# Performance work log

Measured on AMD Instinct MI355X. Metric: run time of the kernel, lower is better.

Reference implementation:

```python
import jax, jax.numpy as jnp
import numpy as np

N_NODES = 100000
N_EDGES = 600000
DIM_IN = 128
DIM_H = 128
DIM_OUT = 64
N_LAYERS = 3
BN_EPS = 1e-5


def setup_inputs() -> dict:
    key = jax.random.key(0)
    ks = jax.random.split(key, 10)
    x = jax.random.normal(ks[0], (N_NODES, DIM_IN), dtype=jnp.float32)
    edge_index = jax.random.randint(ks[1], (2, N_EDGES), 0, N_NODES, dtype=jnp.int64)
    s = 0.05
    conv_w1 = jax.random.normal(ks[2], (N_LAYERS, DIM_H, DIM_H), dtype=jnp.float32) * s
    conv_b1 = jnp.zeros((N_LAYERS, DIM_H), jnp.float32)
    conv_w2 = jax.random.normal(ks[3], (N_LAYERS, DIM_H, DIM_H), dtype=jnp.float32) * s
    conv_b2 = jnp.zeros((N_LAYERS, DIM_H), jnp.float32)
    bn_gamma = jnp.ones((N_LAYERS, DIM_H), jnp.float32)
    bn_beta = jnp.zeros((N_LAYERS, DIM_H), jnp.float32)
    fc1_w = jax.random.normal(ks[4], (DIM_H, DIM_H), dtype=jnp.float32) * s
    fc1_b = jnp.zeros((DIM_H,), jnp.float32)
    fc2_w = jax.random.normal(ks[5], (DIM_H, DIM_OUT), dtype=jnp.float32) * s
    fc2_b = jnp.zeros((DIM_OUT,), jnp.float32)
    # deterministic dropout mask, p=0.5, inverted-dropout scaling baked in (0 or 2)
    dropout_mask = (jax.random.uniform(ks[6], (N_NODES, DIM_H)) < 0.5).astype(jnp.float32) * 2.0
    return {"x": x, "edge_index": edge_index,
            "conv_w1": conv_w1, "conv_b1": conv_b1, "conv_w2": conv_w2, "conv_b2": conv_b2,
            "bn_gamma": bn_gamma, "bn_beta": bn_beta,
            "fc1_w": fc1_w, "fc1_b": fc1_b, "fc2_w": fc2_w, "fc2_b": fc2_b,
            "dropout_mask": dropout_mask}


def reference(x, edge_index, conv_w1, conv_b1, conv_w2, conv_b2,
              bn_gamma, bn_beta, fc1_w, fc1_b, fc2_w, fc2_b, dropout_mask):
    src, dst = edge_index[0], edge_index[1]
    n = x.shape[0]
    h = x
    for l in range(N_LAYERS):
        # GINConv (eps=0): (1+eps)*h + sum_{j->i} h_j, then 2-layer MLP
        agg = h + jax.ops.segment_sum(h[src], dst, num_segments=n)
        z = jnp.maximum(agg @ conv_w1[l] + conv_b1[l], 0.0) @ conv_w2[l] + conv_b2[l]
        z = jnp.maximum(z, 0.0)  # outer ReLU
        # BatchNorm1d (training mode: batch stats, biased variance)
        mean = z.mean(axis=0)
        var = z.var(axis=0)
        h = (z - mean) * jax.lax.rsqrt(var + BN_EPS) * bn_gamma[l] + bn_beta[l]
    h = jnp.maximum(h @ fc1_w + fc1_b, 0.0)
    h = h * dropout_mask  # dropout p=0.5 with precomputed inverted mask
    logits = h @ fc2_w + fc2_b
    return jax.nn.log_softmax(logits, axis=-1)
```

## Files before the change

kernel.cpp:

```cpp
#include <hip/hip_runtime.h>
#include <stdint.h>

#define N_NODES 100000
#define N_EDGES 600000
#define DIM_H   128
#define DIM_OUT 64
#define WPAD    136
#define BN_EPS  1e-5f
#define NBLK    391
#define GRID64_HEAD 1563
#define MLP_GRID 782

typedef __attribute__((ext_vector_type(8))) __bf16        bh8;
typedef __attribute__((ext_vector_type(4))) float         fl4;
typedef __attribute__((ext_vector_type(8))) unsigned short us8;
typedef __attribute__((ext_vector_type(4))) unsigned short us4;

__device__ __forceinline__ unsigned short f2bfbits(float f) {
  unsigned int u = __builtin_bit_cast(unsigned int, f);
  u += 0x7fffu + ((u >> 16) & 1u);
  return (unsigned short)(u >> 16);
}
__device__ __forceinline__ float bf2f(unsigned short b) {
  unsigned int u = ((unsigned int)b) << 16;
  return __builtin_bit_cast(float, u);
}
__device__ __forceinline__ void wave_lds_fence() {
  asm volatile("s_waitcnt lgkmcnt(0)" ::: "memory");
  __builtin_amdgcn_sched_barrier(0);
}

__global__ void prep_kernel(const float* __restrict__ cw1, const float* __restrict__ cw2,
                            const float* __restrict__ fc1w, const float* __restrict__ fc2w,
                            unsigned short* __restrict__ W1F, unsigned short* __restrict__ W2F,
                            unsigned short* __restrict__ F1F, unsigned short* __restrict__ F2F,
                            float* __restrict__ stats, int* __restrict__ deg,
                            unsigned short* __restrict__ zrow) {
  int t = blockIdx.x * 256 + threadIdx.x;
  if (t < 3 * 16384) {
    int l = t >> 14, o = t & 16383;
    int j = o & 7, lane = (o >> 3) & 63, kk = (o >> 9) & 3, n0 = o >> 11;
    int k = kk * 32 + ((lane >> 4) << 3) + j;
    int n = (n0 << 4) + (lane & 15);
    W1F[t] = f2bfbits(cw1[l * 16384 + k * 128 + n]);
    W2F[t] = f2bfbits(cw2[l * 16384 + k * 128 + n]);
  }
  if (t < 16384) {
    int o = t;
    int j = o & 7, lane = (o >> 3) & 63, kk = (o >> 9) & 3, n0 = o >> 11;
    int k = kk * 32 + ((lane >> 4) << 3) + j;
    int n = (n0 << 4) + (lane & 15);
    F1F[t] = f2bfbits(fc1w[k * 128 + n]);
  }
  if (t < 8192) {
    int o = t;
    int j = o & 7, lane = (o >> 3) & 63, kk = (o >> 9) & 3, n0 = o >> 11;
    int k = kk * 32 + ((lane >> 4) << 3) + j;
    int n = (n0 << 4) + (lane & 15);
    F2F[t] = f2bfbits(fc2w[k * 64 + n]);
  }
  if (t < 6144)  stats[t] = 0.f;
  if (t < 128)   zrow[t] = 0;
  if (t < N_NODES) deg[t] = 0;
}

__global__ void deg_xcast(const float* __restrict__ x, unsigned short* __restrict__ xB,
                          const int* __restrict__ ei, int* __restrict__ deg,
                          const float* __restrict__ mask, unsigned int* __restrict__ bmask) {
  int i = blockIdx.x * 256 + threadIdx.x;
  fl4 v = reinterpret_cast<const fl4*>(x)[i];
  us4 p;
#pragma unroll
  for (int j = 0; j < 4; ++j) p[j] = f2bfbits(v[j]);
  reinterpret_cast<us4*>(xB)[i] = p;
  if (i < N_EDGES) atomicAdd(&deg[ei[N_EDGES + i]], 1);
  if (i < N_NODES * 4) {
    const float* mp = mask + (long)i * 32;
    unsigned int b = 0;
#pragma unroll
    for (int j8 = 0; j8 < 8; ++j8) {
      fl4 mv = *reinterpret_cast<const fl4*>(mp + j8 * 4);
      b |= (mv[0] > 0.f ? 1u : 0u) << (j8 * 4 + 0);
      b |= (mv[1] > 0.f ? 1u : 0u) << (j8 * 4 + 1);
      b |= (mv[2] > 0.f ? 1u : 0u) << (j8 * 4 + 2);
      b |= (mv[3] > 0.f ? 1u : 0u) << (j8 * 4 + 3);
    }
    bmask[i] = b;
  }
}

__global__ void scanA(const int* __restrict__ deg, int* __restrict__ rowstart,
                      int* __restrict__ bsum) {
  __shared__ int s[256];
  int t = threadIdx.x, i = blockIdx.x * 256 + t;
  int v = (i < N_NODES) ? deg[i] : 0;
  s[t] = v;
  __syncthreads();
#pragma unroll
  for (int off = 1; off < 256; off <<= 1) {
    int u = (t >= off) ? s[t - off] : 0;
    __syncthreads();
    s[t] += u;
    __syncthreads();
  }
  if (i < N_NODES) rowstart[i] = s[t] - v;
  if (t == 0) bsum[blockIdx.x] = s[255];
}

__global__ void scanC(int* __restrict__ rowstart, const int* __restrict__ bsum,
                      int* __restrict__ cursor) {
  __shared__ int sred[256];
  int b = blockIdx.x, t = threadIdx.x;
  int partial = 0;
  for (int j = t; j < b; j += 256) partial += bsum[j];
  sred[t] = partial;
  __syncthreads();
#pragma unroll
  for (int off = 128; off > 0; off >>= 1) {
    if (t < off) sred[t] += sred[t + off];
    __syncthreads();
  }
  int boffb = sred[0];
  int i = b * 256 + t;
  if (i < N_NODES) {
    int v = rowstart[i] + boffb;
    rowstart[i] = v;
    cursor[i] = v;
  }
  if (i == 0) rowstart[N_NODES] = N_EDGES;
}

__global__ void csr_fill(const int* __restrict__ ei, int* __restrict__ cursor,
                         int* __restrict__ csr_src) {
  int e = blockIdx.x * 256 + threadIdx.x;
  if (e < N_EDGES) {
    int pos = atomicAdd(&cursor[ei[N_EDGES + e]], 1);
    csr_src[pos] = ei[e];
  }
}

__global__ void bn_finalize(const float* __restrict__ stats, const float* __restrict__ gamma,
                            const float* __restrict__ beta, float* __restrict__ sb) {
  int c = threadIdx.x;
  float s = 0.f, ss = 0.f;
#pragma unroll
  for (int r = 0; r < 8; ++r) {
    s  += stats[r * 256 + c];
    ss += stats[r * 256 + 128 + c];
  }
  const float inv_n = 1.0f / (float)N_NODES;
  float mean = s * inv_n;
  float var  = ss * inv_n - mean * mean;
  float sc = gamma[c] * rsqrtf(var + BN_EPS);
  sb[c] = sc;
  sb[128 + c] = beta[c] - mean * sc;
}

template <int AFFINE>
__global__ __launch_bounds__(256)
void gather_h(const unsigned short* __restrict__ H, const float* __restrict__ sb,
              const int* __restrict__ rowstart, const int* __restrict__ csr,
              unsigned short* __restrict__ aggB) {
  int node = blockIdx.x * 4 + (threadIdx.x >> 6);
  int lane = threadIdx.x & 63;
  int q = lane >> 4, lc = lane & 15;
  int c = lc * 8;

  fl4 scA, scB, bcA, bcB;
  if (AFFINE) {
    scA = *reinterpret_cast<const fl4*>(sb + c);
    scB = *reinterpret_cast<const fl4*>(sb + c + 4);
    bcA = *reinterpret_cast<const fl4*>(sb + 128 + c);
    bcB = *reinterpret_cast<const fl4*>(sb + 128 + c + 4);
  }

  int nodeu = __builtin_amdgcn_readfirstlane(node);
  int rs = rowstart[nodeu], re = rowstart[nodeu + 1];
  int cnt = re - rs + 1;
  float acc[8] = {0.f, 0.f, 0.f, 0.f, 0.f, 0.f, 0.f, 0.f};

  for (int base = 0; base < cnt; base += 64) {
    int item = base + lane;
    int myidx = (item == 0) ? nodeu
              : ((item < cnt) ? csr[rs + item - 1] : N_NODES);
    int lim = cnt - base; if (lim > 64) lim = 64;
    for (int sub = 0; sub < lim; sub += 16) {
      int i0 = __shfl(myidx, sub + q);
      int i1 = __shfl(myidx, sub + 4 + q);
      int i2 = __shfl(myidx, sub + 8 + q);
      int i3 = __shfl(myidx, sub + 12 + q);
      us8 r0 = *reinterpret_cast<const us8*>(H + (long)i0 * DIM_H + c);
      us8 r1 = *reinterpret_cast<const us8*>(H + (long)i1 * DIM_H + c);
      us8 r2 = *reinterpret_cast<const us8*>(H + (long)i2 * DIM_H + c);
      us8 r3 = *reinterpret_cast<const us8*>(H + (long)i3 * DIM_H + c);
#pragma unroll
      for (int j = 0; j < 8; ++j)
        acc[j] += (bf2f(r0[j]) + bf2f(r1[j])) + (bf2f(r2[j]) + bf2f(r3[j]));
    }
  }

#pragma unroll
  for (int j = 0; j < 8; ++j) {
    acc[j] += __shfl_xor(acc[j], 16);
    acc[j] += __shfl_xor(acc[j], 32);
  }

  if (q == 0) {
    us8 pk;
    if (AFFINE) {
      float fc = (float)cnt;
#pragma unroll
      for (int j = 0; j < 4; ++j) {
        pk[j]     = f2bfbits(scA[j] * acc[j]     + fc * bcA[j]);
        pk[4 + j] = f2bfbits(scB[j] * acc[4 + j] + fc * bcB[j]);
      }
    } else {
#pragma unroll
      for (int j = 0; j < 8; ++j) pk[j] = f2bfbits(acc[j]);
    }
    *reinterpret_cast<us8*>(aggB + (long)node * DIM_H + c) = pk;
  }
}

__global__ __launch_bounds__(256, 4)
void mlp_kernel(const unsigned short* __restrict__ A,
                const unsigned short* __restrict__ W1F, const float* __restrict__ b1,
                const unsigned short* __restrict__ W2F, const float* __restrict__ b2,
                unsigned short* __restrict__ Z, float* __restrict__ stats) {
  __shared__ __align__(16) unsigned short ybuf[128 * WPAD];
  __shared__ float red[4][2][128];

  const int tid = threadIdx.x;
  const int wid = tid >> 6, lane = tid & 63;
  const int lr = lane & 15, lg = lane >> 4;
  const int row0 = blockIdx.x * 128;

  bh8 afrag[2][4];
#pragma unroll
  for (int rt = 0; rt < 2; ++rt) {
    int row = row0 + wid * 32 + rt * 16 + lr;
    bool valid = row < N_NODES;
    const unsigned short* ap = A + (long)row * DIM_H;
#pragma unroll
    for (int kk = 0; kk < 4; ++kk) {
      us8 t = (us8)0;
      if (valid) t = *reinterpret_cast<const us8*>(ap + kk * 32 + 8 * lg);
      afrag[rt][kk] = __builtin_bit_cast(bh8, t);
    }
  }

  float bias1[8], bias2[8];
#pragma unroll
  for (int n0 = 0; n0 < 8; ++n0) { bias1[n0] = b1[n0 * 16 + lr]; bias2[n0] = b2[n0 * 16 + lr]; }

  bh8 bnxt[4];
#pragma unroll
  for (int kk = 0; kk < 4; ++kk)
    bnxt[kk] = *reinterpret_cast<const bh8*>(&W1F[(kk << 9) + lane * 8]);

#pragma unroll
  for (int n0 = 0; n0 < 8; ++n0) {
    bh8 bc[4];
#pragma unroll
    for (int kk = 0; kk < 4; ++kk) bc[kk] = bnxt[kk];
    if (n0 < 7) {
#pragma unroll
      for (int kk = 0; kk < 4; ++kk)
        bnxt[kk] = *reinterpret_cast<const bh8*>(&W1F[(((n0 + 1) * 4 + kk) << 9) + lane * 8]);
    }
    fl4 acc[2] = {{0,0,0,0},{0,0,0,0}};
#pragma unroll
    for (int kk = 0; kk < 4; ++kk) {
      acc[0] = __builtin_amdgcn_mfma_f32_16x16x32_bf16(afrag[0][kk], bc[kk], acc[0], 0, 0, 0);
      acc[1] = __builtin_amdgcn_mfma_f32_16x16x32_bf16(afrag[1][kk], bc[kk], acc[1], 0, 0, 0);
    }
#pragma unroll
    for (int rt = 0; rt < 2; ++rt)
#pragma unroll
      for (int r = 0; r < 4; ++r) {
        float v = acc[rt][r] + bias1[n0];
        v = v > 0.f ? v : 0.f;
        ybuf[(wid * 32 + rt * 16 + 4 * lg + r) * WPAD + n0 * 16 + lr] = f2bfbits(v);
      }
  }

#pragma unroll
  for (int kk = 0; kk < 4; ++kk)
    bnxt[kk] = *reinterpret_cast<const bh8*>(&W2F[(kk << 9) + lane * 8]);

  wave_lds_fence();

  bh8 a2[2][4];
#pragma unroll
  for (int rt = 0; rt < 2; ++rt)
#pragma unroll
    for (int kk = 0; kk < 4; ++kk)
      a2[rt][kk] = *reinterpret_cast<const bh8*>(
          &ybuf[(wid * 32 + rt * 16 + lr) * WPAD + kk * 32 + 8 * lg]);

  wave_lds_fence();

#pragma unroll
  for (int n0 = 0; n0 < 8; ++n0) {
    bh8 bc[4];
#pragma unroll
    for (int kk = 0; kk < 4; ++kk) bc[kk] = bnxt[kk];
    if (n0 < 7) {
#pragma unroll
      for (int kk = 0; kk < 4; ++kk)
        bnxt[kk] = *reinterpret_cast<const bh8*>(&W2F[(((n0 + 1) * 4 + kk) << 9) + lane * 8]);
    }
    fl4 acc[2] = {{0,0,0,0},{0,0,0,0}};
#pragma unroll
    for (int kk = 0; kk < 4; ++kk) {
      acc[0] = __builtin_amdgcn_mfma_f32_16x16x32_bf16(a2[0][kk], bc[kk], acc[0], 0, 0, 0);
      acc[1] = __builtin_amdgcn_mfma_f32_16x16x32_bf16(a2[1][kk], bc[kk], acc[1], 0, 0, 0);
    }
    float sp = 0.f, qp = 0.f;
#pragma unroll
    for (int rt = 0; rt < 2; ++rt)
#pragma unroll
      for (int r = 0; r < 4; ++r) {
        int row = row0 + wid * 32 + rt * 16 + 4 * lg + r;
        float v = acc[rt][r] + bias2[n0];
        v = v > 0.f ? v : 0.f;
        ybuf[(wid * 32 + rt * 16 + 4 * lg + r) * WPAD + n0 * 16 + lr] = f2bfbits(v);
        if (row < N_NODES) { sp += v; qp += v * v; }
      }
    sp += __shfl_xor(sp, 16); sp += __shfl_xor(sp, 32);
    qp += __shfl_xor(qp, 16); qp += __shfl_xor(qp, 32);
    if (lg == 0) { red[wid][0][n0 * 16 + lr] = sp; red[wid][1][n0 * 16 + lr] = qp; }
  }

  wave_lds_fence();

#pragma unroll
  for (int i = 0; i < 8; ++i) {
    int ch = i * 64 + lane;
    int r  = wid * 32 + (ch >> 4);
    int c8 = (ch & 15) << 3;
    int row = row0 + r;
    if (row < N_NODES)
      *reinterpret_cast<uint4*>(&Z[(long)row * DIM_H + c8]) =
          *reinterpret_cast<const uint4*>(&ybuf[r * WPAD + c8]);
  }

  __syncthreads();

  {
    int which = tid >> 7, cc = tid & 127;
    float v = red[0][which][cc] + red[1][which][cc] + red[2][which][cc] + red[3][which][cc];
    float* dst = stats + (blockIdx.x & 7) * 256;
    unsafeAtomicAdd(&dst[which * 128 + cc], v);
  }
}

__global__ __launch_bounds__(256, 6)
void head_kernel(const unsigned short* __restrict__ Z, const float* __restrict__ sb,
                 const unsigned short* __restrict__ F1F, const float* __restrict__ fc1b,
                 const unsigned short* __restrict__ F2F, const float* __restrict__ fc2b,
                 const unsigned int* __restrict__ bmask, float* __restrict__ out) {
  __shared__ __align__(16) unsigned short ybuf[64 * WPAD];

  const int tid = threadIdx.x;
  const int wid = tid >> 6, lane = tid & 63;
  const int lr = lane & 15, lg = lane >> 4;
  const int row0 = blockIdx.x * 64;

  unsigned int bw[4][4];
#pragma unroll
  for (int r = 0; r < 4; ++r) {
    int row = row0 + wid * 16 + 4 * lg + r;
    if (row < N_NODES) {
      uint4 t = *reinterpret_cast<const uint4*>(bmask + (long)row * 4);
      bw[r][0] = t.x; bw[r][1] = t.y; bw[r][2] = t.z; bw[r][3] = t.w;
    } else {
      bw[r][0] = bw[r][1] = bw[r][2] = bw[r][3] = 0u;
    }
  }

  float bias1[8], bias2[4];
#pragma unroll
  for (int n0 = 0; n0 < 8; ++n0) bias1[n0] = fc1b[n0 * 16 + lr];
#pragma unroll
  for (int n0 = 0; n0 < 4; ++n0) bias2[n0] = fc2b[n0 * 16 + lr];

  bh8 afrag[4];
#pragma unroll
  for (int kk = 0; kk < 4; ++kk) {
    int k0 = kk * 32 + 8 * lg;
    fl4 s0  = *reinterpret_cast<const fl4*>(sb + k0);
    fl4 s1  = *reinterpret_cast<const fl4*>(sb + k0 + 4);
    fl4 bb0 = *reinterpret_cast<const fl4*>(sb + 128 + k0);
    fl4 bb1 = *reinterpret_cast<const fl4*>(sb + 128 + k0 + 4);
    int row = row0 + wid * 16 + lr;
    us8 t = (us8)0;
    if (row < N_NODES) {
      us8 zv = *reinterpret_cast<const us8*>(Z + (long)row * DIM_H + k0);
#pragma unroll
      for (int j = 0; j < 4; ++j) {
        t[j]     = f2bfbits(bf2f(zv[j])     * s0[j] + bb0[j]);
        t[4 + j] = f2bfbits(bf2f(zv[4 + j]) * s1[j] + bb1[j]);
      }
    }
    afrag[kk] = __builtin_bit_cast(bh8, t);
  }

  bh8 bnxt[4];
#pragma unroll
  for (int kk = 0; kk < 4; ++kk)
    bnxt[kk] = *reinterpret_cast<const bh8*>(&F1F[(kk << 9) + lane * 8]);
#pragma unroll
  for (int n0 = 0; n0 < 8; ++n0) {
    bh8 bc[4];
#pragma unroll
    for (int kk = 0; kk < 4; ++kk) bc[kk] = bnxt[kk];
    if (n0 < 7) {
#pragma unroll
      for (int kk = 0; kk < 4; ++kk)
        bnxt[kk] = *reinterpret_cast<const bh8*>(&F1F[(((n0 + 1) * 4 + kk) << 9) + lane * 8]);
    }
    fl4 acc = {0.f, 0.f, 0.f, 0.f};
#pragma unroll
    for (int kk = 0; kk < 4; ++kk)
      acc = __builtin_amdgcn_mfma_f32_16x16x32_bf16(afrag[kk], bc[kk], acc, 0, 0, 0);
#pragma unroll
    for (int r = 0; r < 4; ++r) {
      float v = acc[r] + bias1[n0];
      v = v > 0.f ? v : 0.f;
      float mk = ((bw[r][n0 >> 1] >> (((n0 & 1) << 4) + lr)) & 1u) ? 2.0f : 0.0f;
      ybuf[(wid * 16 + 4 * lg + r) * WPAD + n0 * 16 + lr] = f2bfbits(v * mk);
    }
  }

#pragma unroll
  for (int kk = 0; kk < 4; ++kk)
    bnxt[kk] = *reinterpret_cast<const bh8*>(&F2F[(kk << 9) + lane * 8]);

  wave_lds_fence();

  bh8 a2[4];
#pragma unroll
  for (int kk = 0; kk < 4; ++kk)
    a2[kk] = *reinterpret_cast<const bh8*>(
        &ybuf[(wid * 16 + lr) * WPAD + kk * 32 + 8 * lg]);

  fl4 acc2[4];
#pragma unroll
  for (int n0 = 0; n0 < 4; ++n0) {
    bh8 bc[4];
#pragma unroll
    for (int kk = 0; kk < 4; ++kk) bc[kk] = bnxt[kk];
    if (n0 < 3) {
#pragma unroll
      for (int kk = 0; kk < 4; ++kk)
        bnxt[kk] = *reinterpret_cast<const bh8*>(&F2F[(((n0 + 1) * 4 + kk) << 9) + lane * 8]);
    }
    acc2[n0] = (fl4){0.f, 0.f, 0.f, 0.f};
#pragma unroll
    for (int kk = 0; kk < 4; ++kk)
      acc2[n0] = __builtin_amdgcn_mfma_f32_16x16x32_bf16(a2[kk], bc[kk], acc2[n0], 0, 0, 0);
#pragma unroll
    for (int r = 0; r < 4; ++r) acc2[n0][r] += bias2[n0];
  }

#pragma unroll
  for (int r = 0; r < 4; ++r) {
    float m = fmaxf(fmaxf(acc2[0][r], acc2[1][r]), fmaxf(acc2[2][r], acc2[3][r]));
#pragma unroll
    for (int d = 1; d < 16; d <<= 1) m = fmaxf(m, __shfl_xor(m, d, 16));
    float se = 0.f;
#pragma unroll
    for (int n0 = 0; n0 < 4; ++n0) se += __expf(acc2[n0][r] - m);
#pragma unroll
    for (int d = 1; d < 16; d <<= 1) se += __shfl_xor(se, d, 16);
    float lse = m + __logf(se);
    int row = row0 + wid * 16 + 4 * lg + r;
    if (row < N_NODES) {
#pragma unroll
      for (int n0 = 0; n0 < 4; ++n0)
        out[(long)row * DIM_OUT + n0 * 16 + lr] = acc2[n0][r] - lse;
    }
  }
}

extern "C" void kernel_launch(void* const* d_in, const int* in_sizes, int n_in,
                              void* d_out, int out_size, void* d_ws, size_t ws_size,
                              hipStream_t stream) {
  const float* x      = (const float*)d_in[0];
  const int*   ei     = (const int*)d_in[1];
  const float* cw1    = (const float*)d_in[2];
  const float* cb1    = (const float*)d_in[3];
  const float* cw2    = (const float*)d_in[4];
  const float* cb2    = (const float*)d_in[5];
  const float* gamma  = (const float*)d_in[6];
  const float* beta   = (const float*)d_in[7];
  const float* fc1w   = (const float*)d_in[8];
  const float* fc1b   = (const float*)d_in[9];
  const float* fc2w   = (const float*)d_in[10];
  const float* fc2b   = (const float*)d_in[11];
  const float* mask   = (const float*)d_in[12];
  float* out = (float*)d_out;

  char* ws = (char*)d_ws;
  unsigned short* aggB  = (unsigned short*)ws;
  unsigned short* Zb    = (unsigned short*)(ws + 25600000);
  unsigned short* W1F   = (unsigned short*)(ws + 51200256);
  unsigned short* W2F   = (unsigned short*)(ws + 51298560);
  unsigned short* F1F   = (unsigned short*)(ws + 51396864);
  unsigned short* F2F   = (unsigned short*)(ws + 51429632);
  float*          stats = (float*)(ws + 51446016);
  int*            rowst = (int*)(ws + 51470592);
  int*            cursor= (int*)(ws + 51870596);
  int*            csr   = (int*)(ws + 52270596);
  int*            bsum  = (int*)(ws + 54670596);
  unsigned int*   bmask = (unsigned int*)(ws + 54672160);
  float*          sb    = (float*)(ws + 56272160);
  if (ws_size < 56275232u) return;

  prep_kernel<<<NBLK, 256, 0, stream>>>(cw1, cw2, fc1w, fc2w, W1F, W2F, F1F, F2F,
                                        stats, cursor, Zb + (long)N_NODES * DIM_H);
  deg_xcast<<<12500, 256, 0, stream>>>(x, Zb, ei, cursor, mask, bmask);

  scanA<<<NBLK, 256, 0, stream>>>(cursor, rowst, bsum);
  scanC<<<NBLK, 256, 0, stream>>>(rowst, bsum, cursor);
  csr_fill<<<2344, 256, 0, stream>>>(ei, cursor, csr);

  gather_h<0><<<25000, 256, 0, stream>>>(Zb, nullptr, rowst, csr, aggB);
  mlp_kernel<<<MLP_GRID, 256, 0, stream>>>(aggB, W1F, cb1, W2F, cb2, Zb, stats);
  bn_finalize<<<1, 128, 0, stream>>>(stats, gamma, beta, sb);

  gather_h<1><<<25000, 256, 0, stream>>>(Zb, sb, rowst, csr, aggB);
  mlp_kernel<<<MLP_GRID, 256, 0, stream>>>(aggB, W1F + 16384, cb1 + 128, W2F + 16384,
                                           cb2 + 128, Zb, stats + 2048);
  bn_finalize<<<1, 128, 0, stream>>>(stats + 2048, gamma + 128, beta + 128, sb + 256);

  gather_h<1><<<25000, 256, 0, stream>>>(Zb, sb + 256, rowst, csr, aggB);
  mlp_kernel<<<MLP_GRID, 256, 0, stream>>>(aggB, W1F + 32768, cb1 + 256, W2F + 32768,
                                           cb2 + 256, Zb, stats + 4096);
  bn_finalize<<<1, 128, 0, stream>>>(stats + 4096, gamma + 256, beta + 256, sb + 512);

  head_kernel<<<GRID64_HEAD, 256, 0, stream>>>(Zb, sb + 512,
                                               F1F, fc1b, F2F, fc2b, bmask, out);
}
```

Before: 275.2 us.

## Map four nodes per wave in gather, one node per 16-lane quarter

The gather kernel now assigns four destination nodes to each wavefront, with each 16-lane quarter handling one node's whole neighbour list, instead of one node per wave split across quarters. This removes the cross-quarter shuffle reduction, lets all lanes store, and cuts the grid to a quarter of the blocks. In exchange, quarters loop to the wave's maximum degree, so lanes with shorter lists run padded iterations that read a dummy row.

```diff
diff --git a/kernel.cpp b/kernel.cpp
--- a/kernel.cpp
+++ b/kernel.cpp
@@ -10,6 +10,7 @@
 #define NBLK    391
 #define GRID64_HEAD 1563
 #define MLP_GRID 782
+#define GATHER_GRID 6250
 
 typedef __attribute__((ext_vector_type(8))) __bf16        bh8;
 typedef __attribute__((ext_vector_type(4))) float         fl4;
@@ -161,7 +162,7 @@
 void gather_h(const unsigned short* __restrict__ H, const float* __restrict__ sb,
               const int* __restrict__ rowstart, const int* __restrict__ csr,
               unsigned short* __restrict__ aggB) {
-  int node = blockIdx.x * 4 + (threadIdx.x >> 6);
+  int wbase = (blockIdx.x * 4 + (threadIdx.x >> 6)) * 4;
   int lane = threadIdx.x & 63;
   int q = lane >> 4, lc = lane & 15;
   int c = lc * 8;
@@ -174,21 +175,25 @@
     bcB = *reinterpret_cast<const fl4*>(sb + 128 + c + 4);
   }
 
-  int nodeu = __builtin_amdgcn_readfirstlane(node);
-  int rs = rowstart[nodeu], re = rowstart[nodeu + 1];
+  int nq = wbase + q;
+  int rs = rowstart[nq], re = rowstart[nq + 1];
   int cnt = re - rs + 1;
+  int cmax = cnt;
+  cmax = max(cmax, __shfl_xor(cmax, 16));
+  cmax = max(cmax, __shfl_xor(cmax, 32));
+
   float acc[8] = {0.f, 0.f, 0.f, 0.f, 0.f, 0.f, 0.f, 0.f};
 
-  for (int base = 0; base < cnt; base += 64) {
-    int item = base + lane;
-    int myidx = (item == 0) ? nodeu
+  for (int base = 0; base < cmax; base += 16) {
+    int item = base + lc;
+    int myidx = (item == 0) ? nq
               : ((item < cnt) ? csr[rs + item - 1] : N_NODES);
-    int lim = cnt - base; if (lim > 64) lim = 64;
-    for (int sub = 0; sub < lim; sub += 16) {
-      int i0 = __shfl(myidx, sub + q);
-      int i1 = __shfl(myidx, sub + 4 + q);
-      int i2 = __shfl(myidx, sub + 8 + q);
-      int i3 = __shfl(myidx, sub + 12 + q);
+    int lim = cmax - base; if (lim > 16) lim = 16;
+    for (int m = 0; m < lim; m += 4) {
+      int i0 = __shfl(myidx, (q << 4) + m);
+      int i1 = __shfl(myidx, (q << 4) + m + 1);
+      int i2 = __shfl(myidx, (q << 4) + m + 2);
+      int i3 = __shfl(myidx, (q << 4) + m + 3);
       us8 r0 = *reinterpret_cast<const us8*>(H + (long)i0 * DIM_H + c);
       us8 r1 = *reinterpret_cast<const us8*>(H + (long)i1 * DIM_H + c);
       us8 r2 = *reinterpret_cast<const us8*>(H + (long)i2 * DIM_H + c);
@@ -199,27 +204,19 @@
     }
   }
 
-#pragma unroll
-  for (int j = 0; j < 8; ++j) {
-    acc[j] += __shfl_xor(acc[j], 16);
-    acc[j] += __shfl_xor(acc[j], 32);
-  }
-
-  if (q == 0) {
-    us8 pk;
-    if (AFFINE) {
-      float fc = (float)cnt;
-#pragma unroll
-      for (int j = 0; j < 4; ++j) {
-        pk[j]     = f2bfbits(scA[j] * acc[j]     + fc * bcA[j]);
-        pk[4 + j] = f2bfbits(scB[j] * acc[4 + j] + fc * bcB[j]);
-      }
-    } else {
-#pragma unroll
-      for (int j = 0; j < 8; ++j) pk[j] = f2bfbits(acc[j]);
-    }
-    *reinterpret_cast<us8*>(aggB + (long)node * DIM_H + c) = pk;
-  }
+  us8 pk;
+  if (AFFINE) {
+    float fc = (float)cnt;
+#pragma unroll
+    for (int j = 0; j < 4; ++j) {
+      pk[j]     = f2bfbits(scA[j] * acc[j]     + fc * bcA[j]);
+      pk[4 + j] = f2bfbits(scB[j] * acc[4 + j] + fc * bcB[j]);
+    }
+  } else {
+#pragma unroll
+    for (int j = 0; j < 8; ++j) pk[j] = f2bfbits(acc[j]);
+  }
+  *reinterpret_cast<us8*>(aggB + (long)nq * DIM_H + c) = pk;
 }
 
 __global__ __launch_bounds__(256, 4)
@@ -526,16 +523,16 @@
   scanC<<<NBLK, 256, 0, stream>>>(rowst, bsum, cursor);
   csr_fill<<<2344, 256, 0, stream>>>(ei, cursor, csr);
 
-  gather_h<0><<<25000, 256, 0, stream>>>(Zb, nullptr, rowst, csr, aggB);
+  gather_h<0><<<GATHER_GRID, 256, 0, stream>>>(Zb, nullptr, rowst, csr, aggB);
   mlp_kernel<<<MLP_GRID, 256, 0, stream>>>(aggB, W1F, cb1, W2F, cb2, Zb, stats);
   bn_finalize<<<1, 128, 0, stream>>>(stats, gamma, beta, sb);
 
-  gather_h<1><<<25000, 256, 0, stream>>>(Zb, sb, rowst, csr, aggB);
+  gather_h<1><<<GATHER_GRID, 256, 0, stream>>>(Zb, sb, rowst, csr, aggB);
   mlp_kernel<<<MLP_GRID, 256, 0, stream>>>(aggB, W1F + 16384, cb1 + 128, W2F + 16384,
                                            cb2 + 128, Zb, stats + 2048);
   bn_finalize<<<1, 128, 0, stream>>>(stats + 2048, gamma + 128, beta + 128, sb + 256);
 
-  gather_h<1><<<25000, 256, 0, stream>>>(Zb, sb + 256, rowst, csr, aggB);
+  gather_h<1><<<GATHER_GRID, 256, 0, stream>>>(Zb, sb + 256, rowst, csr, aggB);
   mlp_kernel<<<MLP_GRID, 256, 0, stream>>>(aggB, W1F + 32768, cb1 + 256, W2F + 32768,
                                            cb2 + 256, Zb, stats + 4096);
   bn_finalize<<<1, 128, 0, stream>>>(stats + 4096, gamma + 256, beta + 256, sb + 512);
```

New measurement: 256.7 us, median of 3. 6.7% less time.
